# Kernel optimization log

Hardware: AMD Instinct MI355X
Metric: run time of the kernel (lower is better)

## Reference

```python
import jax, jax.numpy as jnp
import numpy as np

NV = 117000
NE = 468000
EMB = 300
IN_DIM = 768
BATCH = 4096
HID = 500
NUM_LABELS = 2


def setup_inputs() -> dict:
    key = jax.random.key(0)
    ks = jax.random.split(key, 12)
    inp = {
        "input_tensor": jax.random.normal(ks[0], (BATCH, IN_DIM), dtype=jnp.float32),
        "node": jax.random.randint(ks[1], (BATCH,), 0, NV, dtype=jnp.int64),
        "edge_row": jax.random.randint(ks[2], (NE,), 0, NV, dtype=jnp.int32),
        "edge_col": jax.random.randint(ks[3], (NE,), 0, NV, dtype=jnp.int32),
        # learned parameters
        "H0": jax.random.normal(ks[4], (NV, EMB), dtype=jnp.float32) * 1.0,
        "W1": jax.random.normal(ks[5], (EMB, EMB), dtype=jnp.float32) * 0.01,
        "W2": jax.random.normal(ks[6], (EMB, EMB), dtype=jnp.float32) * 0.01,
        "Wa": jax.random.normal(ks[7], (IN_DIM + EMB, HID), dtype=jnp.float32) * 0.03,
        "ba": jnp.zeros((HID,), dtype=jnp.float32),
        "Wb": jax.random.normal(ks[8], (HID, HID), dtype=jnp.float32) * 0.04,
        "bb": jnp.zeros((HID,), dtype=jnp.float32),
        "Wc": jax.random.normal(ks[9], (HID, NUM_LABELS), dtype=jnp.float32) * 0.04,
        "bc": jnp.zeros((NUM_LABELS,), dtype=jnp.float32),
    }
    return inp


def reference(input_tensor, node, edge_row, edge_col, H0, W1, W2, Wa, ba, Wb, bb, Wc, bc):
    nV = H0.shape[0]
    # symmetric normalization D^{-1/2} A D^{-1/2} from edge list (duplicates sum, as in csr)
    deg = jax.ops.segment_sum(jnp.ones_like(edge_row, dtype=H0.dtype), edge_row, num_segments=nV)
    dinv = jnp.where(deg > 0, deg ** -0.5, 0.0)
    vals = dinv[edge_row] * dinv[edge_col]  # [nE]

    def spmm(X):  # LM @ X via gather + segment_sum
        return jax.ops.segment_sum(vals[:, None] * X[edge_col], edge_row, num_segments=nV)

    H1 = jax.nn.sigmoid(spmm(H0 @ W1))        # [nV, EMB]
    H2 = jax.nn.sigmoid(spmm(H1 @ W2))        # [nV, EMB]
    fc = jnp.concatenate([H2[node], input_tensor], axis=1)  # [B, EMB+IN_DIM]
    h = jax.nn.sigmoid(fc @ Wa + ba)
    h = jax.nn.sigmoid(h @ Wb + bb)
    return h @ Wc + bc                        # [B, NUM_LABELS]
```

## Files before the change

### kernel.cpp

```cpp
#include <hip/hip_runtime.h>
#include <hip/hip_bf16.h>

typedef __hip_bfloat16 bf16;

#define NVX 117000
#define NEX 468000
#define EMB 300
#define STR 320
#define IN_DIM 768
#define BATCH 4096
#define HID 500
#define FCK 1088
#define HPAD 512
#define NEB 1829
#define ESL 32

#define CAP1 32768
#define CAP2 4096

#define PRE_W12 (384*STR)
#define PRE_WA  (HPAD*FCK)
#define PRE_WB  (HPAD*HPAD)
#define PRE_TOT (2*PRE_W12 + PRE_WA + PRE_WB)
#define PRE_BLK ((PRE_TOT+255)/256)

typedef __attribute__((ext_vector_type(8))) short frag8;
typedef __attribute__((ext_vector_type(4))) float f32x4;

__device__ __forceinline__ float sigmoidf_(float x){ return 1.0f/(1.0f + __expf(-x)); }
__device__ __forceinline__ float bfs2f(short s){
  return __uint_as_float(((unsigned int)(unsigned short)s) << 16);
}
__device__ __forceinline__ short f2bfs(float f){
  bf16 b = __float2bfloat16(f);
  return *(short*)&b;
}

__device__ __forceinline__ void gload_lds16(const bf16* g, bf16* l){
  __builtin_amdgcn_global_load_lds((const __attribute__((address_space(1))) void*)g,
                                   (__attribute__((address_space(3))) void*)l, 16, 0, 0);
}


__global__ __launch_bounds__(256) void k_setup(const int* __restrict__ erow,
                                               const int* __restrict__ node,
                                               int* __restrict__ deg,
                                               int* __restrict__ flag2,
                                               const float* __restrict__ W1,
                                               const float* __restrict__ W2,
                                               const float* __restrict__ Wa,
                                               const float* __restrict__ Wb,
                                               bf16* __restrict__ Wt1,
                                               bf16* __restrict__ Wt2,
                                               bf16* __restrict__ Wat,
                                               bf16* __restrict__ Wbt){
  long i = (long)blockIdx.x*256 + threadIdx.x;
  if (i < NEX) atomicAdd(&deg[erow[i]], 1);
  if (i < BATCH) flag2[node[i]] = 1;

  if (i < 2*PRE_W12){
    const float* W = (i < PRE_W12) ? W1 : W2;
    bf16* o = (i < PRE_W12) ? Wt1 : Wt2;
    int j = (int)((i < PRE_W12) ? i : i - PRE_W12);
    int n = j / STR, k = j % STR;
    float v = (n < EMB && k < EMB) ? W[k*EMB + n] : 0.0f;
    o[j] = __float2bfloat16(v);
    return;
  }
  i -= 2*PRE_W12;
  if (i < PRE_WA){
    int n = (int)(i / FCK), k = (int)(i % FCK);
    float v = 0.0f;
    if (n < HID){
      if (k < EMB)        v = Wa[(size_t)k*HID + n];
      else if (k >= STR)  v = Wa[(size_t)(k-(STR-EMB))*HID + n];
    }
    Wat[i] = __float2bfloat16(v);
    return;
  }
  i -= PRE_WA;
  if (i < PRE_WB){
    int n = (int)(i / HPAD), k = (int)(i % HPAD);
    float v = (n < HID && k < HID) ? Wb[(size_t)k*HID + n] : 0.0f;
    Wbt[i] = __float2bfloat16(v);
  }
}


__global__ __launch_bounds__(256) void k_flag1c(const int* __restrict__ erow,
                                                const int* __restrict__ ecol,
                                                const int* __restrict__ flag2,
                                                int* __restrict__ flag1,
                                                int* __restrict__ L2,
                                                int* __restrict__ inv2,
                                                int* __restrict__ counts){
  long j = (long)blockIdx.x*256 + threadIdx.x;
  if (j < NEX && flag2[erow[j]]) flag1[ecol[j]] = 1;
  int v = (int)j;
  if (v < NVX && flag2[v]){
    int idx = atomicAdd(&counts[1], 1);
    if (idx < CAP2){ L2[idx] = v; inv2[v] = idx; }
  }
}


__global__ __launch_bounds__(256) void k_edgec(const int* __restrict__ erow,
                                               const int* __restrict__ ecol,
                                               const int* __restrict__ deg,
                                               const int* __restrict__ flag1,
                                               const int* __restrict__ flag2,
                                               int* __restrict__ acnt,
                                               int* __restrict__ scol,
                                               float* __restrict__ sval,
                                               int* __restrict__ L1, int* __restrict__ inv1,
                                               int* __restrict__ counts){
  long j = (long)blockIdx.x*256 + threadIdx.x;
  if (j < NEX){
    int r = erow[j];
    if (flag1[r] | flag2[r]){
      int c = ecol[j];
      int dc = deg[c];
      if (dc > 0){
        float val = rsqrtf((float)deg[r]) * rsqrtf((float)dc);
        int p = atomicAdd(&acnt[r], 1);
        if (p < ESL){
          scol[(size_t)r*ESL + p] = c;
          sval[(size_t)r*ESL + p] = val;
        }
      }
    }
  }
  int v = (int)j;
  if (v < NVX && flag1[v]){
    int idx = atomicAdd(&counts[0], 1);
    if (idx < CAP1){ L1[idx] = v; inv1[v] = idx; }
  }
}


__global__ __launch_bounds__(256) void k_spmm1(const int* __restrict__ acnt,
                                               const int* __restrict__ scol,
                                               const float* __restrict__ sval,
                                               const float* __restrict__ H0,
                                               const int* __restrict__ L1,
                                               const int* __restrict__ counts,
                                               bf16* __restrict__ Gc1){
  int i = (int)((blockIdx.x*blockDim.x + threadIdx.x) >> 6);
  int lane = threadIdx.x & 63;
  if (lane >= 40) return;
  int n1 = counts[0]; if (n1 > CAP1) n1 = CAP1;
  int n1pad = (n1 + 127) & ~127;
  if (i >= n1pad) return;
  int c0 = lane*8;
  bool hv1 = (c0 + 3) < EMB;
  bool hv2 = (c0 + 7) < EMB;
  float acc[8] = {0.f,0.f,0.f,0.f,0.f,0.f,0.f,0.f};
  if (i < n1 && hv1){
    int v = L1[i];
    int ne = acnt[v]; if (ne > ESL) ne = ESL;
    const int*   cp = scol + (size_t)v*ESL;
    const float* vp = sval + (size_t)v*ESL;
    int e = 0;
    for (; e + 3 < ne; e += 4){
      float w0 = vp[e], w1 = vp[e+1], w2 = vp[e+2], w3 = vp[e+3];
      const float* p0 = H0 + (size_t)cp[e  ]*EMB + c0;
      const float* p1 = H0 + (size_t)cp[e+1]*EMB + c0;
      const float* p2 = H0 + (size_t)cp[e+2]*EMB + c0;
      const float* p3 = H0 + (size_t)cp[e+3]*EMB + c0;
      float4 A0 = *(const float4*)p0, B0 = *(const float4*)p1;
      float4 C0 = *(const float4*)p2, D0 = *(const float4*)p3;
      float4 A1, B1, C1, D1;
      if (hv2){
        A1 = *(const float4*)(p0+4); B1 = *(const float4*)(p1+4);
        C1 = *(const float4*)(p2+4); D1 = *(const float4*)(p3+4);
      } else {
        A1 = B1 = C1 = D1 = make_float4(0,0,0,0);
      }
      acc[0] += w0*A0.x + w1*B0.x + w2*C0.x + w3*D0.x;
      acc[1] += w0*A0.y + w1*B0.y + w2*C0.y + w3*D0.y;
      acc[2] += w0*A0.z + w1*B0.z + w2*C0.z + w3*D0.z;
      acc[3] += w0*A0.w + w1*B0.w + w2*C0.w + w3*D0.w;
      acc[4] += w0*A1.x + w1*B1.x + w2*C1.x + w3*D1.x;
      acc[5] += w0*A1.y + w1*B1.y + w2*C1.y + w3*D1.y;
      acc[6] += w0*A1.z + w1*B1.z + w2*C1.z + w3*D1.z;
      acc[7] += w0*A1.w + w1*B1.w + w2*C1.w + w3*D1.w;
    }
    for (; e + 1 < ne; e += 2){
      float va = vp[e], vb = vp[e+1];
      const float* xa = H0 + (size_t)cp[e  ]*EMB + c0;
      const float* xb = H0 + (size_t)cp[e+1]*EMB + c0;
      float4 a0 = *(const float4*)xa;
      float4 b0 = *(const float4*)xb;
      float4 a1 = hv2 ? *(const float4*)(xa+4) : make_float4(0,0,0,0);
      float4 b1 = hv2 ? *(const float4*)(xb+4) : make_float4(0,0,0,0);
      acc[0] += va*a0.x + vb*b0.x;  acc[1] += va*a0.y + vb*b0.y;
      acc[2] += va*a0.z + vb*b0.z;  acc[3] += va*a0.w + vb*b0.w;
      acc[4] += va*a1.x + vb*b1.x;  acc[5] += va*a1.y + vb*b1.y;
      acc[6] += va*a1.z + vb*b1.z;  acc[7] += va*a1.w + vb*b1.w;
    }
    if (e < ne){
      float va = vp[e];
      const float* xa = H0 + (size_t)cp[e]*EMB + c0;
      float4 a0 = *(const float4*)xa;
      float4 a1 = hv2 ? *(const float4*)(xa+4) : make_float4(0,0,0,0);
      acc[0] += va*a0.x; acc[1] += va*a0.y; acc[2] += va*a0.z; acc[3] += va*a0.w;
      acc[4] += va*a1.x; acc[5] += va*a1.y; acc[6] += va*a1.z; acc[7] += va*a1.w;
    }
  }
  frag8 o;
  #pragma unroll
  for (int j=0;j<8;++j) o[j] = f2bfs(acc[j]);
  *(frag8*)(Gc1 + (size_t)i*STR + c0) = o;
}


__global__ __launch_bounds__(256) void k_spmm2(const int* __restrict__ acnt,
                                               const int* __restrict__ scol,
                                               const float* __restrict__ sval,
                                               const bf16* __restrict__ Hc1,
                                               const int* __restrict__ inv1,
                                               const int* __restrict__ L2,
                                               const int* __restrict__ counts,
                                               bf16* __restrict__ Gc2){
  int i = (int)((blockIdx.x*blockDim.x + threadIdx.x) >> 6);
  int lane = threadIdx.x & 63;
  if (lane >= 40) return;
  int n2 = counts[1]; if (n2 > CAP2) n2 = CAP2;
  int n2pad = (n2 + 127) & ~127;
  if (i >= n2pad) return;
  float acc[8] = {0.f,0.f,0.f,0.f,0.f,0.f,0.f,0.f};
  if (i < n2){
    int v = L2[i];
    int ne = acnt[v]; if (ne > ESL) ne = ESL;
    const int*   cp = scol + (size_t)v*ESL;
    const float* vp = sval + (size_t)v*ESL;
    int e = 0;
    for (; e + 1 < ne; e += 2){
      float va = vp[e], vb = vp[e+1];
      frag8 xa = *(const frag8*)(Hc1 + (size_t)inv1[cp[e  ]]*STR + lane*8);
      frag8 xb = *(const frag8*)(Hc1 + (size_t)inv1[cp[e+1]]*STR + lane*8);
      #pragma unroll
      for (int j=0;j<8;++j) acc[j] += va*bfs2f(xa[j]) + vb*bfs2f(xb[j]);
    }
    if (e < ne){
      float va = vp[e];
      frag8 xa = *(const frag8*)(Hc1 + (size_t)inv1[cp[e]]*STR + lane*8);
      #pragma unroll
      for (int j=0;j<8;++j) acc[j] += va*bfs2f(xa[j]);
    }
  }
  frag8 o;
  #pragma unroll
  for (int j=0;j<8;++j) o[j] = f2bfs(acc[j]);
  *(frag8*)(Gc2 + (size_t)i*STR + lane*8) = o;
}


__global__ __launch_bounds__(256) void k_gemm_node(const bf16* __restrict__ A,
                                                   const bf16* __restrict__ Wt,
                                                   bf16* __restrict__ C,
                                                   const int* __restrict__ counts, int which){
  const int row0 = blockIdx.y * 128;
  if (row0 >= counts[which]) return;
  __shared__ bf16 As[128*32];
  __shared__ bf16 Bs[128*32];
  const int tid  = threadIdx.x;
  const int wv   = tid >> 6;
  const int lane = tid & 63;
  const int n0   = blockIdx.x * 128;
  const int wm = wv & 1, wn = wv >> 1;
  const int srow = lane >> 2;
  const int schk = lane & 3;
  const int fr = lane & 15, fq = lane >> 4;

  f32x4 acc[4][4];
  #pragma unroll
  for (int i=0;i<4;++i)
    #pragma unroll
    for (int j=0;j<4;++j) acc[i][j] = (f32x4)(0.0f);

  for (int k0 = 0; k0 < STR; k0 += 32){
    const bf16* ag = A + (size_t)(row0 + wv*16 + srow)*STR + k0 + schk*8;
    gload_lds16(ag,           As + wv*512 + lane*8);
    gload_lds16(ag + 64*STR,  As + 2048 + wv*512 + lane*8);
    const bf16* bg = Wt + (size_t)(n0 + wv*16 + srow)*STR + k0 + schk*8;
    gload_lds16(bg,           Bs + wv*512 + lane*8);
    gload_lds16(bg + 64*STR,  Bs + 2048 + wv*512 + lane*8);
    __syncthreads();
    frag8 a[4], b[4];
    #pragma unroll
    for (int mi=0;mi<4;++mi)
      a[mi] = *(const frag8*)(As + (wm*64 + mi*16 + fr)*32 + fq*8);
    #pragma unroll
    for (int ni=0;ni<4;++ni)
      b[ni] = *(const frag8*)(Bs + (wn*64 + ni*16 + fr)*32 + fq*8);
    #pragma unroll
    for (int mi=0;mi<4;++mi)
      #pragma unroll
      for (int ni=0;ni<4;++ni)
        acc[mi][ni] = __builtin_amdgcn_mfma_f32_16x16x32_bf16(a[mi], b[ni], acc[mi][ni], 0, 0, 0);
    __syncthreads();
  }

  #pragma unroll
  for (int mi=0;mi<4;++mi){
    int row = row0 + wm*64 + mi*16 + fq*4;
    #pragma unroll
    for (int ni=0;ni<4;++ni){
      int col = n0 + wn*64 + ni*16 + fr;
      if (col < STR){
        bf16* cp = C + (size_t)row*STR + col;
        #pragma unroll
        for (int r=0;r<4;++r){
          float v = (col < EMB) ? sigmoidf_(acc[mi][ni][r]) : 0.0f;
          cp[(size_t)r*STR] = __float2bfloat16(v);
        }
      }
    }
  }
}


__global__ __launch_bounds__(256) void k_fc1g(const bf16* __restrict__ Hc2,
                                              const int* __restrict__ node,
                                              const int* __restrict__ inv2,
                                              const float* __restrict__ input,
                                              const bf16* __restrict__ Wat,
                                              const float* __restrict__ ba,
                                              bf16* __restrict__ h1,
                                              float* __restrict__ outp){
  __shared__ bf16 As[128*32];
  __shared__ bf16 Bs[128*32];
  const int tid  = threadIdx.x;
  const int wv   = tid >> 6;
  const int lane = tid & 63;
  const int row0 = blockIdx.y * 128;
  const int n0   = blockIdx.x * 128;
  const int wm = wv & 1, wn = wv >> 1;
  const int srow = lane >> 2;
  const int schk = lane & 3;
  const int fr = lane & 15, fq = lane >> 4;

  if (blockIdx.x == 0 && tid < 256){
    outp[(size_t)row0*2 + tid] = 0.0f;
  }

  const int nlo = inv2[node[row0 + wv*16 + srow]];
  const int nhi = inv2[node[row0 + 64 + wv*16 + srow]];

  f32x4 acc[4][4];
  #pragma unroll
  for (int i=0;i<4;++i)
    #pragma unroll
    for (int j=0;j<4;++j) acc[i][j] = (f32x4)(0.0f);

  for (int k0 = 0; k0 < FCK; k0 += 32){
    if (k0 < STR){
      gload_lds16(Hc2 + (size_t)nlo*STR + k0 + schk*8, As + wv*512 + lane*8);
      gload_lds16(Hc2 + (size_t)nhi*STR + k0 + schk*8, As + 2048 + wv*512 + lane*8);
    } else {
      int c = k0 - STR + schk*8;
      int m0 = wv*16 + srow;
      float4 u0 = *(const float4*)(input + (size_t)(row0+m0)*IN_DIM + c);
      float4 u1 = *(const float4*)(input + (size_t)(row0+m0)*IN_DIM + c + 4);
      frag8 t0;
      t0[0]=f2bfs(u0.x); t0[1]=f2bfs(u0.y); t0[2]=f2bfs(u0.z); t0[3]=f2bfs(u0.w);
      t0[4]=f2bfs(u1.x); t0[5]=f2bfs(u1.y); t0[6]=f2bfs(u1.z); t0[7]=f2bfs(u1.w);
      *(frag8*)(As + m0*32 + schk*8) = t0;
      int m1 = 64 + wv*16 + srow;
      float4 u2 = *(const float4*)(input + (size_t)(row0+m1)*IN_DIM + c);
      float4 u3 = *(const float4*)(input + (size_t)(row0+m1)*IN_DIM + c + 4);
      frag8 t1;
      t1[0]=f2bfs(u2.x); t1[1]=f2bfs(u2.y); t1[2]=f2bfs(u2.z); t1[3]=f2bfs(u2.w);
      t1[4]=f2bfs(u3.x); t1[5]=f2bfs(u3.y); t1[6]=f2bfs(u3.z); t1[7]=f2bfs(u3.w);
      *(frag8*)(As + m1*32 + schk*8) = t1;
    }
    gload_lds16(Wat + (size_t)(n0 + wv*16 + srow)*FCK + k0 + schk*8, Bs + wv*512 + lane*8);
    gload_lds16(Wat + (size_t)(n0 + 64 + wv*16 + srow)*FCK + k0 + schk*8, Bs + 2048 + wv*512 + lane*8);
    __syncthreads();
    frag8 a[4], b[4];
    #pragma unroll
    for (int mi=0;mi<4;++mi)
      a[mi] = *(const frag8*)(As + (wm*64 + mi*16 + fr)*32 + fq*8);
    #pragma unroll
    for (int ni=0;ni<4;++ni)
      b[ni] = *(const frag8*)(Bs + (wn*64 + ni*16 + fr)*32 + fq*8);
    #pragma unroll
    for (int mi=0;mi<4;++mi)
      #pragma unroll
      for (int ni=0;ni<4;++ni)
        acc[mi][ni] = __builtin_amdgcn_mfma_f32_16x16x32_bf16(a[mi], b[ni], acc[mi][ni], 0, 0, 0);
    __syncthreads();
  }

  #pragma unroll
  for (int mi=0;mi<4;++mi){
    int row = row0 + wm*64 + mi*16 + fq*4;
    #pragma unroll
    for (int ni=0;ni<4;++ni){
      int col = n0 + wn*64 + ni*16 + fr;
      float bv = (col < HID) ? ba[col] : 0.0f;
      bf16* cp = h1 + (size_t)row*HPAD + col;
      #pragma unroll
      for (int r=0;r<4;++r)
        cp[(size_t)r*HPAD] = __float2bfloat16(sigmoidf_(acc[mi][ni][r] + bv));
    }
  }
}


__global__ __launch_bounds__(256) void k_fc2o(const bf16* __restrict__ A,
                                              const bf16* __restrict__ B,
                                              const float* __restrict__ bb,
                                              const float* __restrict__ Wc,
                                              const float* __restrict__ bc,
                                              float* __restrict__ out){
  __shared__ bf16 As[128*32];
  __shared__ bf16 Bs[128*32];
  const int tid  = threadIdx.x;
  const int wv   = tid >> 6;
  const int lane = tid & 63;
  const int row0 = blockIdx.y * 128;
  const int n0   = blockIdx.x * 128;
  const int wm = wv & 1, wn = wv >> 1;
  const int srow = lane >> 2;
  const int schk = lane & 3;
  const int fr = lane & 15, fq = lane >> 4;

  f32x4 acc[4][4];
  #pragma unroll
  for (int i=0;i<4;++i)
    #pragma unroll
    for (int j=0;j<4;++j) acc[i][j] = (f32x4)(0.0f);

  for (int k0 = 0; k0 < HPAD; k0 += 32){
    const bf16* ag = A + (size_t)(row0 + wv*16 + srow)*HPAD + k0 + schk*8;
    gload_lds16(ag,            As + wv*512 + lane*8);
    gload_lds16(ag + 64*HPAD,  As + 2048 + wv*512 + lane*8);
    const bf16* bg = B + (size_t)(n0 + wv*16 + srow)*HPAD + k0 + schk*8;
    gload_lds16(bg,            Bs + wv*512 + lane*8);
    gload_lds16(bg + 64*HPAD,  Bs + 2048 + wv*512 + lane*8);
    __syncthreads();
    frag8 a[4], b[4];
    #pragma unroll
    for (int mi=0;mi<4;++mi)
      a[mi] = *(const frag8*)(As + (wm*64 + mi*16 + fr)*32 + fq*8);
    #pragma unroll
    for (int ni=0;ni<4;++ni)
      b[ni] = *(const frag8*)(Bs + (wn*64 + ni*16 + fr)*32 + fq*8);
    #pragma unroll
    for (int mi=0;mi<4;++mi)
      #pragma unroll
      for (int ni=0;ni<4;++ni)
        acc[mi][ni] = __builtin_amdgcn_mfma_f32_16x16x32_bf16(a[mi], b[ni], acc[mi][ni], 0, 0, 0);
    __syncthreads();
  }

  #pragma unroll
  for (int mi=0;mi<4;++mi){
    #pragma unroll
    for (int r=0;r<4;++r){
      int row = row0 + wm*64 + mi*16 + fq*4 + r;
      float s0 = 0.0f, s1 = 0.0f;
      #pragma unroll
      for (int ni=0;ni<4;++ni){
        int col = n0 + wn*64 + ni*16 + fr;
        if (col < HID){
          float v = sigmoidf_(acc[mi][ni][r] + bb[col]);
          s0 += v * Wc[col*2+0];
          s1 += v * Wc[col*2+1];
        }
      }
      #pragma unroll
      for (int off=1; off<16; off<<=1){
        s0 += __shfl_xor(s0, off);
        s1 += __shfl_xor(s1, off);
      }
      if (fr == 0){
        if (n0 == 0 && wn == 0){ s0 += bc[0]; s1 += bc[1]; }
        atomicAdd(out + (size_t)row*2 + 0, s0);
        atomicAdd(out + (size_t)row*2 + 1, s1);
      }
    }
  }
}


extern "C" void kernel_launch(void* const* d_in, const int* in_sizes, int n_in,
                              void* d_out, int out_size, void* d_ws, size_t ws_size,
                              hipStream_t stream){
  const float* input = (const float*)d_in[0];
  const int*   node  = (const int*)d_in[1];
  const int*   erow  = (const int*)d_in[2];
  const int*   ecol  = (const int*)d_in[3];
  const float* H0    = (const float*)d_in[4];
  const float* W1    = (const float*)d_in[5];
  const float* W2    = (const float*)d_in[6];
  const float* Wa    = (const float*)d_in[7];
  const float* ba    = (const float*)d_in[8];
  const float* Wb    = (const float*)d_in[9];
  const float* bb    = (const float*)d_in[10];
  const float* Wc    = (const float*)d_in[11];
  const float* bc    = (const float*)d_in[12];
  float* outp = (float*)d_out;

  char* p = (char*)d_ws;
  auto alloc = [&](size_t bytes)->char*{ char* r = p; p += (bytes + 255) & ~(size_t)255; return r; };
  char* z0     = p;
  int*   deg    = (int*)  alloc((size_t)NVX*4);
  int*   flag1  = (int*)  alloc((size_t)NVX*4);
  int*   flag2  = (int*)  alloc((size_t)NVX*4);
  int*   counts = (int*)  alloc(256);
  int*   acnt   = (int*)  alloc((size_t)NVX*4);
  size_t zlen   = (size_t)(p - z0);
  int*   scol   = (int*)  alloc((size_t)NVX*ESL*4);
  float* sval   = (float*)alloc((size_t)NVX*ESL*4);
  int*   L1     = (int*)  alloc((size_t)CAP1*4);
  int*   inv1   = (int*)  alloc((size_t)NVX*4);
  int*   L2     = (int*)  alloc((size_t)CAP2*4);
  int*   inv2   = (int*)  alloc((size_t)NVX*4);
  bf16*  Gc1    = (bf16*) alloc((size_t)CAP1*STR*2);
  bf16*  Hc1    = (bf16*) alloc((size_t)CAP1*STR*2);
  bf16*  Gc2    = (bf16*) alloc((size_t)CAP2*STR*2);
  bf16*  Hc2    = (bf16*) alloc((size_t)CAP2*STR*2);
  bf16*  Wt1    = (bf16*) alloc((size_t)384*STR*2);
  bf16*  Wt2    = (bf16*) alloc((size_t)384*STR*2);
  bf16*  Wat    = (bf16*) alloc((size_t)HPAD*FCK*2);
  bf16*  Wbt    = (bf16*) alloc((size_t)HPAD*HPAD*2);
  bf16*  h1     = (bf16*) alloc((size_t)BATCH*HPAD*2);

  hipMemsetAsync(z0, 0, zlen, stream);

  k_setup<<<PRE_BLK, 256, 0, stream>>>(erow, node, deg, flag2, W1, W2, Wa, Wb, Wt1, Wt2, Wat, Wbt);
  k_flag1c<<<NEB, 256, 0, stream>>>(erow, ecol, flag2, flag1, L2, inv2, counts);
  k_edgec<<<NEB, 256, 0, stream>>>(erow, ecol, deg, flag1, flag2, acnt, scol, sval,
                                   L1, inv1, counts);

  k_spmm1    <<<CAP1/4, 256, 0, stream>>>(acnt, scol, sval, H0, L1, counts, Gc1);
  k_gemm_node<<<dim3(3, CAP1/128), 256, 0, stream>>>(Gc1, Wt1, Hc1, counts, 0);
  k_spmm2    <<<CAP2/4, 256, 0, stream>>>(acnt, scol, sval, Hc1, inv1, L2, counts, Gc2);
  k_gemm_node<<<dim3(3, CAP2/128), 256, 0, stream>>>(Gc2, Wt2, Hc2, counts, 1);

  k_fc1g<<<dim3(HPAD/128, BATCH/128), 256, 0, stream>>>(Hc2, node, inv2, input, Wat, ba, h1, outp);
  k_fc2o<<<dim3(HPAD/128, BATCH/128), 256, 0, stream>>>(h1, Wbt, bb, Wc, bc, outp);
}
```

Measured before the change: 402.4 us.

## Fuse SpMM gather with dense weight GEMM for both GCN layers

Replaces the separate SpMM and node-GEMM kernels of each layer with one fused kernel per layer. Each block stages its 128 rows' neighbour lists in LDS, gathers and accumulates neighbour features straight into MFMA A-fragments, then multiplies by the full 320-wide weight panel. The weight B-fragments are read directly from global memory. This removes the Gc1/Gc2 intermediate round-trips and two launches. In exchange, each block now holds 20 accumulator tiles, and the GEMM runs with fewer, larger blocks, which may hurt occupancy.

```diff
diff --git a/kernel.cpp b/kernel.cpp
--- a/kernel.cpp
+++ b/kernel.cpp
@@ -14,6 +14,7 @@
 #define HPAD 512
 #define NEB 1829
 #define ESL 32
+#define SLT 33
 
 #define CAP1 32768
 #define CAP2 4096
@@ -138,184 +139,155 @@
 }
 
 
-__global__ __launch_bounds__(256) void k_spmm1(const int* __restrict__ acnt,
-                                               const int* __restrict__ scol,
-                                               const float* __restrict__ sval,
-                                               const float* __restrict__ H0,
-                                               const int* __restrict__ L1,
-                                               const int* __restrict__ counts,
-                                               bf16* __restrict__ Gc1){
-  int i = (int)((blockIdx.x*blockDim.x + threadIdx.x) >> 6);
-  int lane = threadIdx.x & 63;
-  if (lane >= 40) return;
+__global__ __launch_bounds__(512) void k_l1f(const int* __restrict__ acnt,
+                                             const int* __restrict__ scol,
+                                             const float* __restrict__ sval,
+                                             const float* __restrict__ H0,
+                                             const int* __restrict__ L1,
+                                             const int* __restrict__ counts,
+                                             const bf16* __restrict__ Wt1,
+                                             bf16* __restrict__ Hc1){
+  const int row0 = blockIdx.x * 128;
   int n1 = counts[0]; if (n1 > CAP1) n1 = CAP1;
-  int n1pad = (n1 + 127) & ~127;
-  if (i >= n1pad) return;
-  int c0 = lane*8;
-  bool hv1 = (c0 + 3) < EMB;
-  bool hv2 = (c0 + 7) < EMB;
-  float acc[8] = {0.f,0.f,0.f,0.f,0.f,0.f,0.f,0.f};
-  if (i < n1 && hv1){
-    int v = L1[i];
-    int ne = acnt[v]; if (ne > ESL) ne = ESL;
-    const int*   cp = scol + (size_t)v*ESL;
-    const float* vp = sval + (size_t)v*ESL;
-    int e = 0;
-    for (; e + 3 < ne; e += 4){
-      float w0 = vp[e], w1 = vp[e+1], w2 = vp[e+2], w3 = vp[e+3];
-      const float* p0 = H0 + (size_t)cp[e  ]*EMB + c0;
-      const float* p1 = H0 + (size_t)cp[e+1]*EMB + c0;
-      const float* p2 = H0 + (size_t)cp[e+2]*EMB + c0;
-      const float* p3 = H0 + (size_t)cp[e+3]*EMB + c0;
-      float4 A0 = *(const float4*)p0, B0 = *(const float4*)p1;
-      float4 C0 = *(const float4*)p2, D0 = *(const float4*)p3;
-      float4 A1, B1, C1, D1;
-      if (hv2){
-        A1 = *(const float4*)(p0+4); B1 = *(const float4*)(p1+4);
-        C1 = *(const float4*)(p2+4); D1 = *(const float4*)(p3+4);
-      } else {
-        A1 = B1 = C1 = D1 = make_float4(0,0,0,0);
-      }
-      acc[0] += w0*A0.x + w1*B0.x + w2*C0.x + w3*D0.x;
-      acc[1] += w0*A0.y + w1*B0.y + w2*C0.y + w3*D0.y;
-      acc[2] += w0*A0.z + w1*B0.z + w2*C0.z + w3*D0.z;
-      acc[3] += w0*A0.w + w1*B0.w + w2*C0.w + w3*D0.w;
-      acc[4] += w0*A1.x + w1*B1.x + w2*C1.x + w3*D1.x;
-      acc[5] += w0*A1.y + w1*B1.y + w2*C1.y + w3*D1.y;
-      acc[6] += w0*A1.z + w1*B1.z + w2*C1.z + w3*D1.z;
-      acc[7] += w0*A1.w + w1*B1.w + w2*C1.w + w3*D1.w;
-    }
-    for (; e + 1 < ne; e += 2){
-      float va = vp[e], vb = vp[e+1];
-      const float* xa = H0 + (size_t)cp[e  ]*EMB + c0;
-      const float* xb = H0 + (size_t)cp[e+1]*EMB + c0;
-      float4 a0 = *(const float4*)xa;
-      float4 b0 = *(const float4*)xb;
-      float4 a1 = hv2 ? *(const float4*)(xa+4) : make_float4(0,0,0,0);
-      float4 b1 = hv2 ? *(const float4*)(xb+4) : make_float4(0,0,0,0);
-      acc[0] += va*a0.x + vb*b0.x;  acc[1] += va*a0.y + vb*b0.y;
-      acc[2] += va*a0.z + vb*b0.z;  acc[3] += va*a0.w + vb*b0.w;
-      acc[4] += va*a1.x + vb*b1.x;  acc[5] += va*a1.y + vb*b1.y;
-      acc[6] += va*a1.z + vb*b1.z;  acc[7] += va*a1.w + vb*b1.w;
-    }
-    if (e < ne){
-      float va = vp[e];
-      const float* xa = H0 + (size_t)cp[e]*EMB + c0;
-      float4 a0 = *(const float4*)xa;
-      float4 a1 = hv2 ? *(const float4*)(xa+4) : make_float4(0,0,0,0);
-      acc[0] += va*a0.x; acc[1] += va*a0.y; acc[2] += va*a0.z; acc[3] += va*a0.w;
-      acc[4] += va*a1.x; acc[5] += va*a1.y; acc[6] += va*a1.z; acc[7] += va*a1.w;
-    }
-  }
-  frag8 o;
-  #pragma unroll
-  for (int j=0;j<8;++j) o[j] = f2bfs(acc[j]);
-  *(frag8*)(Gc1 + (size_t)i*STR + c0) = o;
-}
-
-
-__global__ __launch_bounds__(256) void k_spmm2(const int* __restrict__ acnt,
-                                               const int* __restrict__ scol,
-                                               const float* __restrict__ sval,
-                                               const bf16* __restrict__ Hc1,
-                                               const int* __restrict__ inv1,
-                                               const int* __restrict__ L2,
-                                               const int* __restrict__ counts,
-                                               bf16* __restrict__ Gc2){
-  int i = (int)((blockIdx.x*blockDim.x + threadIdx.x) >> 6);
-  int lane = threadIdx.x & 63;
-  if (lane >= 40) return;
-  int n2 = counts[1]; if (n2 > CAP2) n2 = CAP2;
-  int n2pad = (n2 + 127) & ~127;
-  if (i >= n2pad) return;
-  float acc[8] = {0.f,0.f,0.f,0.f,0.f,0.f,0.f,0.f};
-  if (i < n2){
-    int v = L2[i];
-    int ne = acnt[v]; if (ne > ESL) ne = ESL;
-    const int*   cp = scol + (size_t)v*ESL;
-    const float* vp = sval + (size_t)v*ESL;
-    int e = 0;
-    for (; e + 1 < ne; e += 2){
-      float va = vp[e], vb = vp[e+1];
-      frag8 xa = *(const frag8*)(Hc1 + (size_t)inv1[cp[e  ]]*STR + lane*8);
-      frag8 xb = *(const frag8*)(Hc1 + (size_t)inv1[cp[e+1]]*STR + lane*8);
-      #pragma unroll
-      for (int j=0;j<8;++j) acc[j] += va*bfs2f(xa[j]) + vb*bfs2f(xb[j]);
-    }
-    if (e < ne){
-      float va = vp[e];
-      frag8 xa = *(const frag8*)(Hc1 + (size_t)inv1[cp[e]]*STR + lane*8);
-      #pragma unroll
-      for (int j=0;j<8;++j) acc[j] += va*bfs2f(xa[j]);
-    }
-  }
-  frag8 o;
-  #pragma unroll
-  for (int j=0;j<8;++j) o[j] = f2bfs(acc[j]);
-  *(frag8*)(Gc2 + (size_t)i*STR + lane*8) = o;
-}
-
-
-__global__ __launch_bounds__(256) void k_gemm_node(const bf16* __restrict__ A,
-                                                   const bf16* __restrict__ Wt,
-                                                   bf16* __restrict__ C,
-                                                   const int* __restrict__ counts, int which){
-  const int row0 = blockIdx.y * 128;
-  if (row0 >= counts[which]) return;
-  __shared__ bf16 As[128*32];
-  __shared__ bf16 Bs[128*32];
-  const int tid  = threadIdx.x;
-  const int wv   = tid >> 6;
+  if (row0 >= n1) return;
+
+  __shared__ int   ecols[128*SLT];
+  __shared__ float evals[128*SLT];
+  __shared__ int   ecnt[128];
+  const int tid = threadIdx.x;
+
+  {
+    int r = tid >> 2, part = tid & 3;
+    int i = row0 + r;
+    int cnt = 0, v = 0;
+    if (i < n1){ v = L1[i]; cnt = acnt[v]; if (cnt > ESL) cnt = ESL; }
+    if (part == 0) ecnt[r] = cnt;
+    int sHi = part*8 + 8; if (sHi > cnt) sHi = cnt;
+    for (int s = part*8; s < sHi; ++s){
+      ecols[r*SLT + s] = scol[(size_t)v*ESL + s];
+      evals[r*SLT + s] = sval[(size_t)v*ESL + s];
+    }
+  }
+  __syncthreads();
+
+  const int wv = tid >> 6;
   const int lane = tid & 63;
-  const int n0   = blockIdx.x * 128;
-  const int wm = wv & 1, wn = wv >> 1;
-  const int srow = lane >> 2;
-  const int schk = lane & 3;
   const int fr = lane & 15, fq = lane >> 4;
-
-  f32x4 acc[4][4];
-  #pragma unroll
-  for (int i=0;i<4;++i)
-    #pragma unroll
-    for (int j=0;j<4;++j) acc[i][j] = (f32x4)(0.0f);
+  const int lr = wv*16 + fr;
+  const int cnt = ecnt[lr];
+
+  f32x4 acc[20];
+  #pragma unroll
+  for (int n=0;n<20;++n) acc[n] = (f32x4)(0.0f);
 
   for (int k0 = 0; k0 < STR; k0 += 32){
-    const bf16* ag = A + (size_t)(row0 + wv*16 + srow)*STR + k0 + schk*8;
-    gload_lds16(ag,           As + wv*512 + lane*8);
-    gload_lds16(ag + 64*STR,  As + 2048 + wv*512 + lane*8);
-    const bf16* bg = Wt + (size_t)(n0 + wv*16 + srow)*STR + k0 + schk*8;
-    gload_lds16(bg,           Bs + wv*512 + lane*8);
-    gload_lds16(bg + 64*STR,  Bs + 2048 + wv*512 + lane*8);
-    __syncthreads();
-    frag8 a[4], b[4];
-    #pragma unroll
-    for (int mi=0;mi<4;++mi)
-      a[mi] = *(const frag8*)(As + (wm*64 + mi*16 + fr)*32 + fq*8);
-    #pragma unroll
-    for (int ni=0;ni<4;++ni)
-      b[ni] = *(const frag8*)(Bs + (wn*64 + ni*16 + fr)*32 + fq*8);
-    #pragma unroll
-    for (int mi=0;mi<4;++mi)
-      #pragma unroll
-      for (int ni=0;ni<4;++ni)
-        acc[mi][ni] = __builtin_amdgcn_mfma_f32_16x16x32_bf16(a[mi], b[ni], acc[mi][ni], 0, 0, 0);
-    __syncthreads();
-  }
-
-  #pragma unroll
-  for (int mi=0;mi<4;++mi){
-    int row = row0 + wm*64 + mi*16 + fq*4;
-    #pragma unroll
-    for (int ni=0;ni<4;++ni){
-      int col = n0 + wn*64 + ni*16 + fr;
-      if (col < STR){
-        bf16* cp = C + (size_t)row*STR + col;
-        #pragma unroll
-        for (int r=0;r<4;++r){
-          float v = (col < EMB) ? sigmoidf_(acc[mi][ni][r]) : 0.0f;
-          cp[(size_t)r*STR] = __float2bfloat16(v);
+    const int base = k0 + fq*8;
+    float g[8] = {0.f,0.f,0.f,0.f,0.f,0.f,0.f,0.f};
+    if (base < EMB){
+      const bool full = (base + 8) <= EMB;
+      for (int e = 0; e < cnt; ++e){
+        float vv = evals[lr*SLT + e];
+        const float* hp = H0 + (size_t)ecols[lr*SLT + e]*EMB + base;
+        float4 x0 = *(const float4*)hp;
+        g[0] += vv*x0.x; g[1] += vv*x0.y; g[2] += vv*x0.z; g[3] += vv*x0.w;
+        if (full){
+          float4 x1 = *(const float4*)(hp + 4);
+          g[4] += vv*x1.x; g[5] += vv*x1.y; g[6] += vv*x1.z; g[7] += vv*x1.w;
         }
       }
+    }
+    frag8 a;
+    #pragma unroll
+    for (int j=0;j<8;++j) a[j] = f2bfs(g[j]);
+    #pragma unroll
+    for (int n=0;n<20;++n){
+      frag8 b = *(const frag8*)(Wt1 + (size_t)(n*16 + fr)*STR + base);
+      acc[n] = __builtin_amdgcn_mfma_f32_16x16x32_bf16(a, b, acc[n], 0, 0, 0);
+    }
+  }
+
+  #pragma unroll
+  for (int n=0;n<20;++n){
+    int col = n*16 + fr;
+    bf16* cp = Hc1 + (size_t)(row0 + wv*16 + fq*4)*STR + col;
+    #pragma unroll
+    for (int r=0;r<4;++r){
+      float v = (col < EMB) ? sigmoidf_(acc[n][r]) : 0.0f;
+      cp[(size_t)r*STR] = __float2bfloat16(v);
+    }
+  }
+}
+
+
+__global__ __launch_bounds__(512) void k_l2f(const int* __restrict__ acnt,
+                                             const int* __restrict__ scol,
+                                             const float* __restrict__ sval,
+                                             const bf16* __restrict__ Hc1,
+                                             const int* __restrict__ inv1,
+                                             const int* __restrict__ L2,
+                                             const int* __restrict__ counts,
+                                             const bf16* __restrict__ Wt2,
+                                             bf16* __restrict__ Hc2){
+  const int row0 = blockIdx.x * 128;
+  int n2 = counts[1]; if (n2 > CAP2) n2 = CAP2;
+  if (row0 >= n2) return;
+
+  __shared__ int   ecols[128*SLT];
+  __shared__ float evals[128*SLT];
+  __shared__ int   ecnt[128];
+  const int tid = threadIdx.x;
+
+  {
+    int r = tid >> 2, part = tid & 3;
+    int i = row0 + r;
+    int cnt = 0, v = 0;
+    if (i < n2){ v = L2[i]; cnt = acnt[v]; if (cnt > ESL) cnt = ESL; }
+    if (part == 0) ecnt[r] = cnt;
+    int sHi = part*8 + 8; if (sHi > cnt) sHi = cnt;
+    for (int s = part*8; s < sHi; ++s){
+      ecols[r*SLT + s] = inv1[scol[(size_t)v*ESL + s]];
+      evals[r*SLT + s] = sval[(size_t)v*ESL + s];
+    }
+  }
+  __syncthreads();
+
+  const int wv = tid >> 6;
+  const int lane = tid & 63;
+  const int fr = lane & 15, fq = lane >> 4;
+  const int lr = wv*16 + fr;
+  const int cnt = ecnt[lr];
+
+  f32x4 acc[20];
+  #pragma unroll
+  for (int n=0;n<20;++n) acc[n] = (f32x4)(0.0f);
+
+  for (int k0 = 0; k0 < STR; k0 += 32){
+    const int base = k0 + fq*8;
+    float g[8] = {0.f,0.f,0.f,0.f,0.f,0.f,0.f,0.f};
+    for (int e = 0; e < cnt; ++e){
+      float vv = evals[lr*SLT + e];
+      frag8 x = *(const frag8*)(Hc1 + (size_t)ecols[lr*SLT + e]*STR + base);
+      #pragma unroll
+      for (int j=0;j<8;++j) g[j] += vv*bfs2f(x[j]);
+    }
+    frag8 a;
+    #pragma unroll
+    for (int j=0;j<8;++j) a[j] = f2bfs(g[j]);
+    #pragma unroll
+    for (int n=0;n<20;++n){
+      frag8 b = *(const frag8*)(Wt2 + (size_t)(n*16 + fr)*STR + base);
+      acc[n] = __builtin_amdgcn_mfma_f32_16x16x32_bf16(a, b, acc[n], 0, 0, 0);
+    }
+  }
+
+  #pragma unroll
+  for (int n=0;n<20;++n){
+    int col = n*16 + fr;
+    bf16* cp = Hc2 + (size_t)(row0 + wv*16 + fq*4)*STR + col;
+    #pragma unroll
+    for (int r=0;r<4;++r){
+      float v = (col < EMB) ? sigmoidf_(acc[n][r]) : 0.0f;
+      cp[(size_t)r*STR] = __float2bfloat16(v);
     }
   }
 }
@@ -519,9 +491,7 @@
   int*   inv1   = (int*)  alloc((size_t)NVX*4);
   int*   L2     = (int*)  alloc((size_t)CAP2*4);
   int*   inv2   = (int*)  alloc((size_t)NVX*4);
-  bf16*  Gc1    = (bf16*) alloc((size_t)CAP1*STR*2);
   bf16*  Hc1    = (bf16*) alloc((size_t)CAP1*STR*2);
-  bf16*  Gc2    = (bf16*) alloc((size_t)CAP2*STR*2);
   bf16*  Hc2    = (bf16*) alloc((size_t)CAP2*STR*2);
   bf16*  Wt1    = (bf16*) alloc((size_t)384*STR*2);
   bf16*  Wt2    = (bf16*) alloc((size_t)384*STR*2);
@@ -536,10 +506,8 @@
   k_edgec<<<NEB, 256, 0, stream>>>(erow, ecol, deg, flag1, flag2, acnt, scol, sval,
                                    L1, inv1, counts);
 
-  k_spmm1    <<<CAP1/4, 256, 0, stream>>>(acnt, scol, sval, H0, L1, counts, Gc1);
-  k_gemm_node<<<dim3(3, CAP1/128), 256, 0, stream>>>(Gc1, Wt1, Hc1, counts, 0);
-  k_spmm2    <<<CAP2/4, 256, 0, stream>>>(acnt, scol, sval, Hc1, inv1, L2, counts, Gc2);
-  k_gemm_node<<<dim3(3, CAP2/128), 256, 0, stream>>>(Gc2, Wt2, Hc2, counts, 1);
+  k_l1f<<<CAP1/128, 512, 0, stream>>>(acnt, scol, sval, H0, L1, counts, Wt1, Hc1);
+  k_l2f<<<CAP2/128, 512, 0, stream>>>(acnt, scol, sval, Hc1, inv1, L2, counts, Wt2, Hc2);
 
   k_fc1g<<<dim3(HPAD/128, BATCH/128), 256, 0, stream>>>(Hc2, node, inv2, input, Wat, ba, h1, outp);
   k_fc2o<<<dim3(HPAD/128, BATCH/128), 256, 0, stream>>>(h1, Wbt, bb, Wc, bc, outp);
```

Result: slower. 567.9 us (+41.1%).
